# Kernel tuning notes

Measured on AMD Instinct MI355X. Metric: run time of the kernel, lower is better.

## Reference

```python
import jax, jax.numpy as jnp
import numpy as np

B, T, IN_DIM, H, C = 2048, 512, 28, 64, 10


def setup_inputs() -> dict:
    key = jax.random.key(0)
    ks = jax.random.split(key, 7)
    s = 1.0 / np.sqrt(H)  # PyTorch RNN init scale
    u = lambda k, shape: jax.random.uniform(k, shape, jnp.float32, -s, s)
    return {
        "x": jax.random.normal(ks[0], (B, 1, T, IN_DIM), jnp.float32),
        "W_ih": u(ks[1], (3 * H, IN_DIM)),  # gates ordered (r, z, n)
        "W_hh": u(ks[2], (3 * H, H)),
        "b_ih": u(ks[3], (3 * H,)),
        "b_hh": u(ks[4], (3 * H,)),
        "W_out": u(ks[5], (C, H)),
        "b_out": u(ks[6], (C,)),
    }


def reference(x, W_ih, W_hh, b_ih, b_hh, W_out, b_out):
    x = x[:, 0]  # squeeze(1) -> [B, T, IN]
    # Precompute all input-to-gate projections once: [B, T, 3H]
    xg = jnp.einsum("bti,gi->btg", x, W_ih) + b_ih

    def step(h, xg_t):
        gh = h @ W_hh.T + b_hh                      # [B, 3H]
        xr, xz, xn = jnp.split(xg_t, 3, axis=-1)
        hr, hz, hn = jnp.split(gh, 3, axis=-1)
        r = jax.nn.sigmoid(xr + hr)
        z = jax.nn.sigmoid(xz + hz)
        n = jnp.tanh(xn + r * hn)
        h_new = (1.0 - z) * n + z * h
        return h_new, None

    h0 = jnp.zeros((x.shape[0], H), x.dtype)
    hT, _ = jax.lax.scan(step, h0, jnp.swapaxes(xg, 0, 1))  # scan over time
    logits = hT @ W_out.T + b_out                            # [B, C]
    return jax.nn.softmax(logits, axis=-1)
```

## Files before the change

kernel.cpp:

```cpp
#include <hip/hip_runtime.h>

#define BB     2048
#define TT     512
#define INDIM  28
#define HH     64
#define NC     10
#define ROWS   16
#define NTHREADS 256
#define LDH    104

typedef __attribute__((ext_vector_type(8))) _Float16 f16x8;
typedef __attribute__((ext_vector_type(4))) _Float16 f16x4;
typedef __attribute__((ext_vector_type(4))) float     f32x4;

__device__ __forceinline__ float frcp(float v)  { return __builtin_amdgcn_rcpf(v); }
__device__ __forceinline__ float fsig(float v)  { return frcp(1.f + __expf(-v)); }
__device__ __forceinline__ float ftanh_(float v){ return fmaf(-2.f, frcp(1.f + __expf(2.f*v)), 1.f); }

#define MFMA(A_, B_, C_) __builtin_amdgcn_mfma_f32_16x16x32_f16((A_), (B_), (C_), 0, 0, 0)

__device__ __forceinline__ void lds_barrier() {
    asm volatile("s_waitcnt lgkmcnt(0)" ::: "memory");
    __builtin_amdgcn_s_barrier();
}

__device__ __forceinline__ f16x8 cvt_x8(const float4 a, const float4 b) {
    f16x8 r;
    r[0] = (_Float16)a.x; r[1] = (_Float16)a.y; r[2] = (_Float16)a.z; r[3] = (_Float16)a.w;
    r[4] = (_Float16)b.x; r[5] = (_Float16)b.y; r[6] = (_Float16)b.z; r[7] = (_Float16)b.w;
    return r;
}

extern "C" __global__ __launch_bounds__(NTHREADS, 1)
void gru_mfma(const float* __restrict__ x,
              const float* __restrict__ W_ih,
              const float* __restrict__ W_hh,
              const float* __restrict__ b_ih,
              const float* __restrict__ b_hh,
              const float* __restrict__ W_out,
              const float* __restrict__ b_out,
              float* __restrict__ out)
{
    __shared__ __align__(16) _Float16 H_[2][16][LDH];
    __shared__ float hs_f[ROWS][HH];
    __shared__ float lg[ROWS][NC];

    const int tid = threadIdx.x;
    const int w   = tid >> 6;
    const int l   = tid & 63;
    const int c   = l & 15;
    const int hi  = l >> 4;
    const int hi8 = hi * 8;
    const int u   = w * 16 + c;
    const int u0  = w * 16 + 4 * hi;
    const int r0  = blockIdx.x * ROWS;

    f16x8 Bh[9];
    {
        const int GS[9][2] = {{0,0},{0,1},{0,2},{1,0},{1,1},{1,2},{2,0},{2,1},{3,2}};
        #pragma unroll
        for (int f = 0; f < 9; ++f) {
            const int g = GS[f][0], s = GS[f][1];
            #pragma unroll
            for (int j = 0; j < 8; ++j) {
                const int k = s * 32 + hi8 + j;
                float v = 0.f;
                if (g == 2)      { if (k < 64) v = W_hh[(size_t)(u + 128) * HH + k]; }
                else if (g == 3) { if (k >= 64 && k < 64 + INDIM) v = W_ih[(size_t)(u + 128) * INDIM + (k - 64)]; }
                else {
                    const int ru = u + 64 * g;
                    if (k < 64)              v = W_hh[(size_t)ru * HH + k];
                    else if (k < 64 + INDIM) v = W_ih[(size_t)ru * INDIM + (k - 64)];
                }
                Bh[f][j] = (_Float16)v;
            }
        }
    }
    f32x4 bv_r, bv_z, bv_nh, bv_nx;
    #pragma unroll
    for (int i = 0; i < 4; ++i) {
        bv_r[i]  = b_ih[u0 + i]       + b_hh[u0 + i];
        bv_z[i]  = b_ih[u0 + i + 64]  + b_hh[u0 + i + 64];
        bv_nh[i] = b_hh[u0 + i + 128];
        bv_nx[i] = b_ih[u0 + i + 128];
    }

    for (int i = tid; i < 2 * 16 * LDH; i += NTHREADS) ((_Float16*)H_)[i] = (_Float16)0.f;

    const float* xlane = x + (size_t)(r0 + c) * (size_t)TT * INDIM + hi8;
    const float4 zf4 = {0.f, 0.f, 0.f, 0.f};
    const bool xfull = (hi < 3);
    float4 xa[8], xb[8];
    #pragma unroll
    for (int k = 0; k < 8; ++k) {
        xa[k] = *(const float4*)(xlane + (size_t)k * INDIM);
        xb[k] = xfull ? *(const float4*)(xlane + (size_t)k * INDIM + 4) : zf4;
    }
    __syncthreads();

    float h[4] = {0.f, 0.f, 0.f, 0.f};
    f16x8 xf = cvt_x8(xa[0], xb[0]);
    int p = 0;

    const float* xnext = xlane + (size_t)8 * INDIM;

    for (int g = 0; g < TT / 8; ++g) {
        const bool more = (g + 1) < (TT / 8);
        #pragma unroll
        for (int k = 0; k < 8; ++k) {
            const f16x8 bf0 = *(const f16x8*)&H_[p][c][hi8];
            const f16x8 bf1 = *(const f16x8*)&H_[p][c][32 + hi8];

            f32x4 a0 = MFMA(Bh[2], xf, bv_r);
            f32x4 a1 = MFMA(Bh[5], xf, bv_z);
            f32x4 a3 = MFMA(Bh[8], xf, bv_nx);
            f32x4 a2 = MFMA(Bh[6], bf0, bv_nh);
            a0 = MFMA(Bh[0], bf0, a0);
            a1 = MFMA(Bh[3], bf0, a1);
            a2 = MFMA(Bh[7], bf1, a2);
            a0 = MFMA(Bh[1], bf1, a0);
            a1 = MFMA(Bh[4], bf1, a1);

            f16x4 hv;
            #pragma unroll
            for (int i = 0; i < 4; ++i) {
                const float rg = fsig(a0[i]);
                const float zg = fsig(a1[i]);
                const float ng = ftanh_(fmaf(rg, a2[i], a3[i]));
                h[i] = fmaf(zg, h[i] - ng, ng);
                hv[i] = (_Float16)h[i];
            }
            *(f16x4*)&H_[p ^ 1][c][u0] = hv;

            if (more) {
                xa[k] = *(const float4*)(xnext + (size_t)k * INDIM);
                if (xfull) xb[k] = *(const float4*)(xnext + (size_t)k * INDIM + 4);
            }
            xf = cvt_x8(xa[(k + 1) & 7], xb[(k + 1) & 7]);

            lds_barrier();
            p ^= 1;
        }
        xnext += (size_t)8 * INDIM;
    }

    #pragma unroll
    for (int i = 0; i < 4; ++i) hs_f[c][u0 + i] = h[i];
    __syncthreads();
    if (tid < ROWS * NC) {
        const int rr = tid / NC, cc = tid % NC;
        float s = b_out[cc];
        const float* wo = W_out + (size_t)cc * HH;
        #pragma unroll
        for (int j = 0; j < HH; ++j) s = fmaf(wo[j], hs_f[rr][j], s);
        lg[rr][cc] = s;
    }
    __syncthreads();
    if (tid < ROWS) {
        float mx = -1e30f;
        #pragma unroll
        for (int cc = 0; cc < NC; ++cc) mx = fmaxf(mx, lg[tid][cc]);
        float e[NC]; float ssum = 0.f;
        #pragma unroll
        for (int cc = 0; cc < NC; ++cc) { e[cc] = __expf(lg[tid][cc] - mx); ssum += e[cc]; }
        const float inv = 1.f / ssum;
        float* op = out + (size_t)(r0 + tid) * NC;
        #pragma unroll
        for (int cc = 0; cc < NC; ++cc) op[cc] = e[cc] * inv;
    }
}

extern "C" void kernel_launch(void* const* d_in, const int* in_sizes, int n_in,
                              void* d_out, int out_size, void* d_ws, size_t ws_size,
                              hipStream_t stream) {
    const float* x     = (const float*)d_in[0];
    const float* W_ih  = (const float*)d_in[1];
    const float* W_hh  = (const float*)d_in[2];
    const float* b_ih  = (const float*)d_in[3];
    const float* b_hh  = (const float*)d_in[4];
    const float* W_out = (const float*)d_in[5];
    const float* b_out = (const float*)d_in[6];
    (void)in_sizes; (void)n_in; (void)d_ws; (void)ws_size; (void)out_size;

    gru_mfma<<<BB / ROWS, NTHREADS, 0, stream>>>(x, W_ih, W_hh, b_ih, b_hh,
                                                 W_out, b_out, (float*)d_out);
}
```

Measured before the change: 187.1 us.

## Duplicate MFMA work across two wave halves to split gate nonlinearities

Doubles the block to 512 threads. Each pair of waves redundantly computes the same MFMA gate products, and each half then evaluates the sigmoid/tanh update for only two of the four output rows, which halves the per-wave transcendental chain on the serial critical path. It also switches the x float-to-half conversion to packed cvt_pkrtz, which rounds toward zero instead of to nearest. The costs are doubled MFMA work per block, more waves contending for the barrier each step, and a register budget bounded by launch_bounds(512,2).

```diff
diff --git a/kernel.cpp b/kernel.cpp
--- a/kernel.cpp
+++ b/kernel.cpp
@@ -6,11 +6,12 @@
 #define HH     64
 #define NC     10
 #define ROWS   16
-#define NTHREADS 256
+#define NTHREADS 512
 #define LDH    104
 
 typedef __attribute__((ext_vector_type(8))) _Float16 f16x8;
-typedef __attribute__((ext_vector_type(4))) _Float16 f16x4;
+typedef __attribute__((ext_vector_type(2))) _Float16 f16x2;
+typedef __attribute__((ext_vector_type(2))) __fp16   fp16x2;
 typedef __attribute__((ext_vector_type(4))) float     f32x4;
 
 __device__ __forceinline__ float frcp(float v)  { return __builtin_amdgcn_rcpf(v); }
@@ -25,13 +26,15 @@
 }
 
 __device__ __forceinline__ f16x8 cvt_x8(const float4 a, const float4 b) {
-    f16x8 r;
-    r[0] = (_Float16)a.x; r[1] = (_Float16)a.y; r[2] = (_Float16)a.z; r[3] = (_Float16)a.w;
-    r[4] = (_Float16)b.x; r[5] = (_Float16)b.y; r[6] = (_Float16)b.z; r[7] = (_Float16)b.w;
-    return r;
-}
-
-extern "C" __global__ __launch_bounds__(NTHREADS, 1)
+    union { fp16x2 p[4]; f16x8 v; } U;
+    U.p[0] = __builtin_amdgcn_cvt_pkrtz(a.x, a.y);
+    U.p[1] = __builtin_amdgcn_cvt_pkrtz(a.z, a.w);
+    U.p[2] = __builtin_amdgcn_cvt_pkrtz(b.x, b.y);
+    U.p[3] = __builtin_amdgcn_cvt_pkrtz(b.z, b.w);
+    return U.v;
+}
+
+extern "C" __global__ __launch_bounds__(NTHREADS, 2)
 void gru_mfma(const float* __restrict__ x,
               const float* __restrict__ W_ih,
               const float* __restrict__ W_hh,
@@ -45,15 +48,17 @@
     __shared__ float hs_f[ROWS][HH];
     __shared__ float lg[ROWS][NC];
 
-    const int tid = threadIdx.x;
-    const int w   = tid >> 6;
-    const int l   = tid & 63;
-    const int c   = l & 15;
-    const int hi  = l >> 4;
-    const int hi8 = hi * 8;
-    const int u   = w * 16 + c;
-    const int u0  = w * 16 + 4 * hi;
-    const int r0  = blockIdx.x * ROWS;
+    const int tid  = threadIdx.x;
+    const int wave = tid >> 6;
+    const int wq   = wave & 3;
+    const int half = wave >> 2;
+    const int l    = tid & 63;
+    const int c    = l & 15;
+    const int hi   = l >> 4;
+    const int hi8  = hi * 8;
+    const int u    = wq * 16 + c;
+    const int u0   = wq * 16 + 4 * hi;
+    const int r0   = blockIdx.x * ROWS;
 
     f16x8 Bh[9];
     {
@@ -98,7 +103,7 @@
     }
     __syncthreads();
 
-    float h[4] = {0.f, 0.f, 0.f, 0.f};
+    float h0 = 0.f, h1 = 0.f;
     f16x8 xf = cvt_x8(xa[0], xb[0]);
     int p = 0;
 
@@ -121,16 +126,27 @@
             a0 = MFMA(Bh[1], bf1, a0);
             a1 = MFMA(Bh[4], bf1, a1);
 
-            f16x4 hv;
-            #pragma unroll
-            for (int i = 0; i < 4; ++i) {
-                const float rg = fsig(a0[i]);
-                const float zg = fsig(a1[i]);
-                const float ng = ftanh_(fmaf(rg, a2[i], a3[i]));
-                h[i] = fmaf(zg, h[i] - ng, ng);
-                hv[i] = (_Float16)h[i];
+            f16x2 hv;
+            if (half == 0) {
+                {   const float rg = fsig(a0[0]);
+                    const float zg = fsig(a1[0]);
+                    const float ng = ftanh_(fmaf(rg, a2[0], a3[0]));
+                    h0 = fmaf(zg, h0 - ng, ng); hv[0] = (_Float16)h0; }
+                {   const float rg = fsig(a0[1]);
+                    const float zg = fsig(a1[1]);
+                    const float ng = ftanh_(fmaf(rg, a2[1], a3[1]));
+                    h1 = fmaf(zg, h1 - ng, ng); hv[1] = (_Float16)h1; }
+            } else {
+                {   const float rg = fsig(a0[2]);
+                    const float zg = fsig(a1[2]);
+                    const float ng = ftanh_(fmaf(rg, a2[2], a3[2]));
+                    h0 = fmaf(zg, h0 - ng, ng); hv[0] = (_Float16)h0; }
+                {   const float rg = fsig(a0[3]);
+                    const float zg = fsig(a1[3]);
+                    const float ng = ftanh_(fmaf(rg, a2[3], a3[3]));
+                    h1 = fmaf(zg, h1 - ng, ng); hv[1] = (_Float16)h1; }
             }
-            *(f16x4*)&H_[p ^ 1][c][u0] = hv;
+            *(f16x2*)&H_[p ^ 1][c][u0 + 2 * half] = hv;
 
             if (more) {
                 xa[k] = *(const float4*)(xnext + (size_t)k * INDIM);
@@ -144,8 +160,8 @@
         xnext += (size_t)8 * INDIM;
     }
 
-    #pragma unroll
-    for (int i = 0; i < 4; ++i) hs_f[c][u0 + i] = h[i];
+    hs_f[c][u0 + 2 * half]     = h0;
+    hs_f[c][u0 + 2 * half + 1] = h1;
     __syncthreads();
     if (tid < ROWS * NC) {
         const int rr = tid / NC, cc = tid % NC;
```

Result: slower. 238.4 us (+27.4%).
